# Kernel optimization log

Hardware: AMD Instinct MI355X
Metric: run time of the kernel (lower is better)

## Reference

```python
import jax, jax.numpy as jnp
import numpy as np

KERNEL_MUL = 10.0
KERNEL_NUM = 5


def _multi_kernel(dist, n_samples):
    # bandwidth estimated from detached distances (torch uses .data)
    bw = jax.lax.stop_gradient(jnp.sum(dist)) / (n_samples * n_samples - n_samples)
    bw = bw / (KERNEL_MUL ** (KERNEL_NUM // 2))
    k = jnp.zeros_like(dist)
    for i in range(KERNEL_NUM):
        k = k + jnp.exp(-dist / (bw * KERNEL_MUL ** i))
    return k


def setup_inputs() -> dict:
    key = jax.random.key(0)
    k1, k2 = jax.random.split(key)
    B, D = 256, 512
    source = jax.random.normal(k1, (B, D), dtype=jnp.float32)
    target = jax.random.normal(k2, (B, D), dtype=jnp.float32)
    return {"source": source, "target": target}


def reference(source, target):
    B = source.shape[0]
    src = source.reshape(B, -1)
    tgt = target.reshape(target.shape[0], -1)
    total = jnp.concatenate([src, tgt], axis=0)  # [N, D], N = 2B
    N = total.shape[0]

    # L2 pairwise distances via norm expansion (avoids [N,N,D] intermediate)
    sq = jnp.sum(total * total, axis=1)  # [N]
    L2 = jnp.maximum(sq[:, None] + sq[None, :] - 2.0 * (total @ total.T), 0.0)

    # L1 pairwise distances (structurally needs pairwise diffs)
    L1 = jnp.sum(jnp.abs(total[:, None, :] - total[None, :, :]), axis=-1)  # [N, N]

    kernels = _multi_kernel(L2, N) + _multi_kernel(L1, N)

    XX = kernels[:B, :B]
    YY = kernels[B:, B:]
    XY = kernels[:B, B:]
    YX = kernels[B:, :B]
    return jnp.mean(XX + YY - XY - YX)
```

## Files before the change

### kernel.cpp

```cpp
#include <hip/hip_runtime.h>
#include <hip/hip_fp16.h>

#define NROWS 512
#define BHALF 256
#define DIM   512
#define TILE  64
#define DCHUNK 64
#define NCHUNK 8
#define NN (NROWS * NROWS)
#define SOFF (8 * NN)

#define ACC(A, Bb, IV, JV)                                    \
    {                                                         \
        const float d_ = (IV) - (JV);                         \
        a2[A][Bb] = fmaf(d_, d_, a2[A][Bb]);                  \
        a1[A][Bb] += fabsf(d_);                               \
    }

#define STEP(DD)                                              \
    {                                                         \
        const float4 ivv = *(const float4*)&ai[DD][ty4];      \
        const float4 jvv = *(const float4*)&aj[DD][tx4];      \
        ACC(0, 0, ivv.x, jvv.x) ACC(0, 1, ivv.x, jvv.y)       \
        ACC(0, 2, ivv.x, jvv.z) ACC(0, 3, ivv.x, jvv.w)       \
        ACC(1, 0, ivv.y, jvv.x) ACC(1, 1, ivv.y, jvv.y)       \
        ACC(1, 2, ivv.y, jvv.z) ACC(1, 3, ivv.y, jvv.w)       \
        ACC(2, 0, ivv.z, jvv.x) ACC(2, 1, ivv.z, jvv.y)       \
        ACC(2, 2, ivv.z, jvv.z) ACC(2, 3, ivv.z, jvv.w)       \
        ACC(3, 0, ivv.w, jvv.x) ACC(3, 1, ivv.w, jvv.y)       \
        ACC(3, 2, ivv.w, jvv.z) ACC(3, 3, ivv.w, jvv.w)       \
    }

__device__ __forceinline__ unsigned int pack_h2(float l2v, float l1v) {
    const __half2 h = __halves2half2(__float2half_rn(l2v), __float2half_rn(l1v));
    union { __half2 h; unsigned int u; } c; c.h = h;
    return c.u;
}

__global__ __launch_bounds__(256) void k_dist(const float* __restrict__ src,
                                              const float* __restrict__ tgt,
                                              float* __restrict__ ws,
                                              float* __restrict__ out)
{
    __shared__ float ai[DCHUNK][TILE];
    __shared__ float aj[DCHUNK][TILE];

    const int tj = blockIdx.x;
    const int ti = blockIdx.y;
    const int dc = blockIdx.z;
    const int t  = threadIdx.x;

    if (t == 0 && tj == 0 && ti == 0 && dc == 0) out[0] = 0.0f;

    {
        const int r  = t & 63;
        const int dg = t >> 6;
        const int gi = ti * TILE + r;
        const int gj = tj * TILE + r;
        const float* prow_i = (gi < BHALF ? src + (size_t)gi * DIM
                                          : tgt + (size_t)(gi - BHALF) * DIM) + dc * DCHUNK;
        const float* prow_j = (gj < BHALF ? src + (size_t)gj * DIM
                                          : tgt + (size_t)(gj - BHALF) * DIM) + dc * DCHUNK;
#pragma unroll
        for (int k = 0; k < 4; ++k) {
            const int d4 = dg * 4 + k;
            const float4 vi = *(const float4*)(prow_i + d4 * 4);
            const float4 vj = *(const float4*)(prow_j + d4 * 4);
            ai[d4 * 4 + 0][r] = vi.x; ai[d4 * 4 + 1][r] = vi.y;
            ai[d4 * 4 + 2][r] = vi.z; ai[d4 * 4 + 3][r] = vi.w;
            aj[d4 * 4 + 0][r] = vj.x; aj[d4 * 4 + 1][r] = vj.y;
            aj[d4 * 4 + 2][r] = vj.z; aj[d4 * 4 + 3][r] = vj.w;
        }
    }
    __syncthreads();

    const int tx  = t & 15;
    const int ty  = t >> 4;
    const int tx4 = tx * 4;
    const int ty4 = ty * 4;

    float a2[4][4], a1[4][4];
#pragma unroll
    for (int a = 0; a < 4; ++a)
#pragma unroll
        for (int b = 0; b < 4; ++b) { a2[a][b] = 0.f; a1[a][b] = 0.f; }

#pragma unroll 4
    for (int d = 0; d < DCHUNK; d += 2) {
        STEP(d)
        STEP(d + 1)
    }

    unsigned int* part = (unsigned int*)ws + (size_t)dc * NN;
    const int gj0 = tj * TILE + tx4;
#pragma unroll
    for (int a = 0; a < 4; ++a) {
        const int gi = ti * TILE + ty4 + a;
        const uint4 pk = make_uint4(pack_h2(a2[a][0], a1[a][0]),
                                    pack_h2(a2[a][1], a1[a][1]),
                                    pack_h2(a2[a][2], a1[a][2]),
                                    pack_h2(a2[a][3], a1[a][3]));
        *(uint4*)&part[(size_t)gi * NROWS + gj0] = pk;
    }

    float s2 = 0.f, s1 = 0.f;
#pragma unroll
    for (int a = 0; a < 4; ++a)
#pragma unroll
        for (int b = 0; b < 4; ++b) { s2 += a2[a][b]; s1 += a1[a][b]; }
#pragma unroll
    for (int off = 32; off > 0; off >>= 1) {
        s2 += __shfl_down(s2, off);
        s1 += __shfl_down(s1, off);
    }
    __syncthreads();
    float* red = &ai[0][0];
    const int wave = t >> 6;
    if ((t & 63) == 0) { red[wave * 2] = s2; red[wave * 2 + 1] = s1; }
    __syncthreads();
    if (t == 0) {
        const int bid = (dc * 8 + ti) * 8 + tj;
        ws[SOFF + bid]       = red[0] + red[2] + red[4] + red[6];
        ws[SOFF + 512 + bid] = red[1] + red[3] + red[5] + red[7];
    }
}

__global__ __launch_bounds__(256) void k_mmd(const float* __restrict__ ws,
                                             float* __restrict__ out)
{
    const int t = threadIdx.x;
    __shared__ float sred[8];

    float sp2 = ws[SOFF + t] + ws[SOFF + 256 + t];
    float sp1 = ws[SOFF + 512 + t] + ws[SOFF + 768 + t];
#pragma unroll
    for (int off = 32; off > 0; off >>= 1) {
        sp2 += __shfl_down(sp2, off);
        sp1 += __shfl_down(sp1, off);
    }
    if ((t & 63) == 0) { sred[(t >> 6) * 2] = sp2; sred[(t >> 6) * 2 + 1] = sp1; }
    __syncthreads();
    const float S2 = sred[0] + sred[2] + sred[4] + sred[6];
    const float S1 = sred[1] + sred[3] + sred[5] + sred[7];
    const float r2 = 26163200.0f / S2;
    const float r1 = 26163200.0f / S1;

    const __half2* part = (const __half2*)ws;

    float acc = 0.f;
    const int base = blockIdx.x * 1024 + t;
#pragma unroll
    for (int q = 0; q < 4; ++q) {
        const int idx = base + q * 256;
        float l2 = 0.f, l1 = 0.f;
#pragma unroll
        for (int c = 0; c < NCHUNK; ++c) {
            const float2 f = __half22float2(part[(size_t)c * NN + idx]);
            l2 += f.x;
            l1 += f.y;
        }
        float kv = 0.f;
        float f2 = r2, f1 = r1;
#pragma unroll
        for (int tt = 0; tt < 5; ++tt) {
            kv += __expf(-l2 * f2) + __expf(-l1 * f1);
            f2 *= 0.1f;
            f1 *= 0.1f;
        }
        const int i = idx >> 9;
        const int j = idx & 511;
        const float sgn = (((i ^ j) & BHALF) == 0) ? 1.0f : -1.0f;
        acc += sgn * kv;
    }
#pragma unroll
    for (int off = 32; off > 0; off >>= 1) acc += __shfl_down(acc, off);

    __syncthreads();
    if ((t & 63) == 0) sred[t >> 6] = acc;
    __syncthreads();
    if (t == 0) {
        const float s = sred[0] + sred[1] + sred[2] + sred[3];
        atomicAdd(out, s * (1.0f / 65536.0f));
    }
}

extern "C" void kernel_launch(void* const* d_in, const int* in_sizes, int n_in,
                              void* d_out, int out_size, void* d_ws, size_t ws_size,
                              hipStream_t stream)
{
    const float* src = (const float*)d_in[0];
    const float* tgt = (const float*)d_in[1];
    float* ws  = (float*)d_ws;
    float* out = (float*)d_out;

    dim3 g1(8, 8, 8);
    k_dist<<<g1, 256, 0, stream>>>(src, tgt, ws, out);
    k_mmd<<<256, 256, 0, stream>>>(ws, out);
}
```

Baseline: 78.55 us.

## Enlarge distance tiles to 128x128 with 4x8 outputs per thread

Retiles the pairwise-distance kernel to 128x128 output tiles with 512 threads, each thread computing a 4x8 micro-tile. The shared-memory operands for the next step are prefetched into registers. The dimension chunk is halved to 32, so there are twice as many chunks, which keeps the block count at 256. The goal is more arithmetic per shared-memory load and better latency hiding. The cost is double the fp16 partial-distance traffic, which k_dist writes and k_mmd reads back and sums, plus higher register pressure.

```diff
diff --git a/kernel.cpp b/kernel.cpp
--- a/kernel.cpp
+++ b/kernel.cpp
@@ -4,32 +4,24 @@
 #define NROWS 512
 #define BHALF 256
 #define DIM   512
-#define TILE  64
-#define DCHUNK 64
-#define NCHUNK 8
+#define TI    128
+#define DC    32
+#define NCHUNK 16
 #define NN (NROWS * NROWS)
-#define SOFF (8 * NN)
-
-#define ACC(A, Bb, IV, JV)                                    \
+#define SOFF (NCHUNK * NN)
+
+#define PAIR(A, B, IV, JV)                                    \
     {                                                         \
         const float d_ = (IV) - (JV);                         \
-        a2[A][Bb] = fmaf(d_, d_, a2[A][Bb]);                  \
-        a1[A][Bb] += fabsf(d_);                               \
-    }
-
-#define STEP(DD)                                              \
-    {                                                         \
-        const float4 ivv = *(const float4*)&ai[DD][ty4];      \
-        const float4 jvv = *(const float4*)&aj[DD][tx4];      \
-        ACC(0, 0, ivv.x, jvv.x) ACC(0, 1, ivv.x, jvv.y)       \
-        ACC(0, 2, ivv.x, jvv.z) ACC(0, 3, ivv.x, jvv.w)       \
-        ACC(1, 0, ivv.y, jvv.x) ACC(1, 1, ivv.y, jvv.y)       \
-        ACC(1, 2, ivv.y, jvv.z) ACC(1, 3, ivv.y, jvv.w)       \
-        ACC(2, 0, ivv.z, jvv.x) ACC(2, 1, ivv.z, jvv.y)       \
-        ACC(2, 2, ivv.z, jvv.z) ACC(2, 3, ivv.z, jvv.w)       \
-        ACC(3, 0, ivv.w, jvv.x) ACC(3, 1, ivv.w, jvv.y)       \
-        ACC(3, 2, ivv.w, jvv.z) ACC(3, 3, ivv.w, jvv.w)       \
-    }
+        a2[A][B] = fmaf(d_, d_, a2[A][B]);                    \
+        a1[A][B] += fabsf(d_);                                \
+    }
+
+#define ROW(A, IVC)                                           \
+    PAIR(A, 0, IVC, jva.x) PAIR(A, 1, IVC, jva.y)             \
+    PAIR(A, 2, IVC, jva.z) PAIR(A, 3, IVC, jva.w)             \
+    PAIR(A, 4, IVC, jvb.x) PAIR(A, 5, IVC, jvb.y)             \
+    PAIR(A, 6, IVC, jvb.z) PAIR(A, 7, IVC, jvb.w)
 
 __device__ __forceinline__ unsigned int pack_h2(float l2v, float l1v) {
     const __half2 h = __halves2half2(__float2half_rn(l2v), __float2half_rn(l1v));
@@ -37,13 +29,13 @@
     return c.u;
 }
 
-__global__ __launch_bounds__(256) void k_dist(const float* __restrict__ src,
-                                              const float* __restrict__ tgt,
-                                              float* __restrict__ ws,
-                                              float* __restrict__ out)
+__global__ __launch_bounds__(512, 2) void k_dist(const float* __restrict__ src,
+                                                 const float* __restrict__ tgt,
+                                                 float* __restrict__ ws,
+                                                 float* __restrict__ out)
 {
-    __shared__ float ai[DCHUNK][TILE];
-    __shared__ float aj[DCHUNK][TILE];
+    __shared__ float ai[DC][TI];
+    __shared__ float aj[DC][TI];
 
     const int tj = blockIdx.x;
     const int ti = blockIdx.y;
@@ -53,61 +45,73 @@
     if (t == 0 && tj == 0 && ti == 0 && dc == 0) out[0] = 0.0f;
 
     {
-        const int r  = t & 63;
-        const int dg = t >> 6;
-        const int gi = ti * TILE + r;
-        const int gj = tj * TILE + r;
-        const float* prow_i = (gi < BHALF ? src + (size_t)gi * DIM
-                                          : tgt + (size_t)(gi - BHALF) * DIM) + dc * DCHUNK;
-        const float* prow_j = (gj < BHALF ? src + (size_t)gj * DIM
-                                          : tgt + (size_t)(gj - BHALF) * DIM) + dc * DCHUNK;
+        const int r2   = t & 255;
+        const int half = t >> 8;
+        const int isJ  = r2 >> 7;
+        const int rr   = r2 & 127;
+        const int grow = (isJ ? tj : ti) * TI + rr;
+        const float* prow = (grow < BHALF ? src + (size_t)grow * DIM
+                                          : tgt + (size_t)(grow - BHALF) * DIM)
+                            + dc * DC + half * 16;
+        float (*dst)[TI] = isJ ? aj : ai;
 #pragma unroll
         for (int k = 0; k < 4; ++k) {
-            const int d4 = dg * 4 + k;
-            const float4 vi = *(const float4*)(prow_i + d4 * 4);
-            const float4 vj = *(const float4*)(prow_j + d4 * 4);
-            ai[d4 * 4 + 0][r] = vi.x; ai[d4 * 4 + 1][r] = vi.y;
-            ai[d4 * 4 + 2][r] = vi.z; ai[d4 * 4 + 3][r] = vi.w;
-            aj[d4 * 4 + 0][r] = vj.x; aj[d4 * 4 + 1][r] = vj.y;
-            aj[d4 * 4 + 2][r] = vj.z; aj[d4 * 4 + 3][r] = vj.w;
-        }
-    }
-    __syncthreads();
-
-    const int tx  = t & 15;
-    const int ty  = t >> 4;
-    const int tx4 = tx * 4;
-    const int ty4 = ty * 4;
-
-    float a2[4][4], a1[4][4];
+            const float4 v = *(const float4*)(prow + k * 4);
+            const int d0 = half * 16 + k * 4;
+            dst[d0 + 0][rr] = v.x; dst[d0 + 1][rr] = v.y;
+            dst[d0 + 2][rr] = v.z; dst[d0 + 3][rr] = v.w;
+        }
+    }
+    __syncthreads();
+
+    const int jx  = t & 15;
+    const int iy  = t >> 4;
+    const int jx4 = jx * 4;
+    const int iy4 = iy * 4;
+
+    float a2[4][8], a1[4][8];
 #pragma unroll
     for (int a = 0; a < 4; ++a)
 #pragma unroll
-        for (int b = 0; b < 4; ++b) { a2[a][b] = 0.f; a1[a][b] = 0.f; }
-
+        for (int b = 0; b < 8; ++b) { a2[a][b] = 0.f; a1[a][b] = 0.f; }
+
+    float4 iv  = *(const float4*)&ai[0][iy4];
+    float4 jva = *(const float4*)&aj[0][jx4];
+    float4 jvb = *(const float4*)&aj[0][jx4 + 64];
 #pragma unroll 4
-    for (int d = 0; d < DCHUNK; d += 2) {
-        STEP(d)
-        STEP(d + 1)
-    }
-
-    unsigned int* part = (unsigned int*)ws + (size_t)dc * NN;
-    const int gj0 = tj * TILE + tx4;
+    for (int d = 0; d < DC; ++d) {
+        float4 niv, nja, njb;
+        if (d + 1 < DC) {
+            niv = *(const float4*)&ai[d + 1][iy4];
+            nja = *(const float4*)&aj[d + 1][jx4];
+            njb = *(const float4*)&aj[d + 1][jx4 + 64];
+        }
+        ROW(0, iv.x) ROW(1, iv.y) ROW(2, iv.z) ROW(3, iv.w)
+        if (d + 1 < DC) { iv = niv; jva = nja; jvb = njb; }
+    }
+
+    unsigned int* part_w = (unsigned int*)ws + (size_t)dc * NN;
+    const int gj0 = tj * TI + jx4;
 #pragma unroll
     for (int a = 0; a < 4; ++a) {
-        const int gi = ti * TILE + ty4 + a;
-        const uint4 pk = make_uint4(pack_h2(a2[a][0], a1[a][0]),
-                                    pack_h2(a2[a][1], a1[a][1]),
-                                    pack_h2(a2[a][2], a1[a][2]),
-                                    pack_h2(a2[a][3], a1[a][3]));
-        *(uint4*)&part[(size_t)gi * NROWS + gj0] = pk;
+        const int gi = ti * TI + iy4 + a;
+        const uint4 pk0 = make_uint4(pack_h2(a2[a][0], a1[a][0]),
+                                     pack_h2(a2[a][1], a1[a][1]),
+                                     pack_h2(a2[a][2], a1[a][2]),
+                                     pack_h2(a2[a][3], a1[a][3]));
+        const uint4 pk1 = make_uint4(pack_h2(a2[a][4], a1[a][4]),
+                                     pack_h2(a2[a][5], a1[a][5]),
+                                     pack_h2(a2[a][6], a1[a][6]),
+                                     pack_h2(a2[a][7], a1[a][7]));
+        *(uint4*)&part_w[(size_t)gi * NROWS + gj0]      = pk0;
+        *(uint4*)&part_w[(size_t)gi * NROWS + gj0 + 64] = pk1;
     }
 
     float s2 = 0.f, s1 = 0.f;
 #pragma unroll
     for (int a = 0; a < 4; ++a)
 #pragma unroll
-        for (int b = 0; b < 4; ++b) { s2 += a2[a][b]; s1 += a1[a][b]; }
+        for (int b = 0; b < 8; ++b) { s2 += a2[a][b]; s1 += a1[a][b]; }
 #pragma unroll
     for (int off = 32; off > 0; off >>= 1) {
         s2 += __shfl_down(s2, off);
@@ -119,9 +123,12 @@
     if ((t & 63) == 0) { red[wave * 2] = s2; red[wave * 2 + 1] = s1; }
     __syncthreads();
     if (t == 0) {
-        const int bid = (dc * 8 + ti) * 8 + tj;
-        ws[SOFF + bid]       = red[0] + red[2] + red[4] + red[6];
-        ws[SOFF + 512 + bid] = red[1] + red[3] + red[5] + red[7];
+        const int bid = (dc * 4 + ti) * 4 + tj;
+        float r2s = 0.f, r1s = 0.f;
+#pragma unroll
+        for (int w = 0; w < 8; ++w) { r2s += red[w * 2]; r1s += red[w * 2 + 1]; }
+        ws[SOFF + bid]       = r2s;
+        ws[SOFF + 512 + bid] = r1s;
     }
 }
 
@@ -131,8 +138,8 @@
     const int t = threadIdx.x;
     __shared__ float sred[8];
 
-    float sp2 = ws[SOFF + t] + ws[SOFF + 256 + t];
-    float sp1 = ws[SOFF + 512 + t] + ws[SOFF + 768 + t];
+    float sp2 = ws[SOFF + t];
+    float sp1 = ws[SOFF + 512 + t];
 #pragma unroll
     for (int off = 32; off > 0; off >>= 1) {
         sp2 += __shfl_down(sp2, off);
@@ -193,7 +200,7 @@
     float* ws  = (float*)d_ws;
     float* out = (float*)d_out;
 
-    dim3 g1(8, 8, 8);
-    k_dist<<<g1, 256, 0, stream>>>(src, tgt, ws, out);
+    dim3 g1(4, 4, 16);
+    k_dist<<<g1, 512, 0, stream>>>(src, tgt, ws, out);
     k_mmd<<<256, 256, 0, stream>>>(ws, out);
 }
```

New measurement: 82.34 us. 1.05x slower.
